# Performance work log

Measured on AMD Instinct MI355X. Metric: run time of the kernel, lower is better.

## Reference

```python
import jax, jax.numpy as jnp
import numpy as np

N_NODES = 100_000
N_EDGES = 1_600_000
HID = 64
TXT = 384
N_LAYERS = 2
BATCH = 1024


def setup_inputs() -> dict:
    key = jax.random.key(0)
    ks = jax.random.split(key, 13)
    s = 0.05
    return {
        "text_emb": jax.random.normal(ks[0], (N_NODES, TXT), dtype=jnp.float32),
        "weights": jax.random.uniform(ks[1], (N_EDGES,), dtype=jnp.float32),
        "W_enc": jax.random.normal(ks[2], (TXT, HID), dtype=jnp.float32) * s,
        "b_enc": jax.random.normal(ks[3], (HID,), dtype=jnp.float32) * s,
        "Wself_f": jax.random.normal(ks[4], (N_LAYERS, HID, HID), dtype=jnp.float32) * s,
        "Wneigh_f": jax.random.normal(ks[5], (N_LAYERS, HID, HID), dtype=jnp.float32) * s,
        "b_f": jax.random.normal(ks[6], (N_LAYERS, HID), dtype=jnp.float32) * s,
        "Wself_r": jax.random.normal(ks[7], (N_LAYERS, HID, HID), dtype=jnp.float32) * s,
        "Wneigh_r": jax.random.normal(ks[8], (N_LAYERS, HID, HID), dtype=jnp.float32) * s,
        "b_r": jax.random.normal(ks[9], (N_LAYERS, HID), dtype=jnp.float32) * s,
        "src": jax.random.randint(ks[10], (N_EDGES,), 0, N_NODES, dtype=jnp.int32),
        "dst": jax.random.randint(ks[11], (N_EDGES,), 0, N_NODES, dtype=jnp.int32),
        "ids_idx": jax.random.randint(ks[12], (BATCH,), 0, N_NODES, dtype=jnp.int32),
    }


def _inv_degree(idx, n, e_dtype):
    deg = jax.ops.segment_sum(jnp.ones((idx.shape[0],), dtype=e_dtype), idx, num_segments=n)
    return jnp.where(deg > 0, 1.0 / deg, 0.0)  # zero in-degree -> 0 (DGL mean)


def _sage_mean(x, src, dst, w, inv_deg, Wself, Wneigh, b):
    # DGL SAGEConv('mean') with edge_weight: neigh = mean_over_in_edges(w * h_src)
    m = w[:, None] * x[src]                                   # [E, H] gather
    neigh = jax.ops.segment_sum(m, dst, num_segments=x.shape[0]) * inv_deg[:, None]
    return x @ Wself + neigh @ Wneigh + b


def reference(text_emb, weights, W_enc, b_enc, Wself_f, Wneigh_f, b_f,
              Wself_r, Wneigh_r, b_r, src, dst, ids_idx):
    n = text_emb.shape[0]
    inv_f = _inv_degree(dst, n, text_emb.dtype)   # forward graph: aggregate into dst
    inv_r = _inv_degree(src, n, text_emb.dtype)   # reversed graph: aggregate into src
    x = text_emb @ W_enc + b_enc                  # text encoder
    for l in range(Wself_f.shape[0]):
        y = jax.nn.relu(_sage_mean(x, src, dst, weights, inv_f,
                                   Wself_f[l], Wneigh_f[l], b_f[l]))
        y = y + jax.nn.relu(_sage_mean(x, dst, src, weights, inv_r,
                                       Wself_r[l], Wneigh_r[l], b_r[l]))
        x = x + y                                 # skip connection
    feat = x[ids_idx]                             # [B, H]
    return feat / jnp.linalg.norm(feat, axis=1, keepdims=True)
```

## Files before the change

kernel.cpp:

```cpp
#include <hip/hip_runtime.h>

#define NN 100000
#define NE 1600000
#define HID 64
#define TXT 384
#define BATCH 1024
#define NBUCK 391
#define SBLK 256
#define EPB ((NE + SBLK - 1) / SBLK)
#define LDK2 72
#define EB2 782

typedef __attribute__((ext_vector_type(8))) short short8;
typedef __attribute__((ext_vector_type(4))) float float4v;

__device__ __forceinline__ ushort f2bf(float f) {
  unsigned u = __float_as_uint(f);
  unsigned r = (u + 0x7fffu + ((u >> 16) & 1u)) >> 16;
  return (ushort)r;
}
__device__ __forceinline__ float bf2f(ushort u) {
  return __uint_as_float(((unsigned)u) << 16);
}
__device__ __forceinline__ short8 pack8(float4 a, float4 b) {
  short8 s;
  s[0] = (short)f2bf(a.x); s[1] = (short)f2bf(a.y);
  s[2] = (short)f2bf(a.z); s[3] = (short)f2bf(a.w);
  s[4] = (short)f2bf(b.x); s[5] = (short)f2bf(b.y);
  s[6] = (short)f2bf(b.z); s[7] = (short)f2bf(b.w);
  return s;
}

__device__ __forceinline__ int scan_incl(int v, int* lds8) {
  const int lane = threadIdx.x & 63, wv = threadIdx.x >> 6;
  const int nw = blockDim.x >> 6;
  #pragma unroll
  for (int d = 1; d < 64; d <<= 1) {
    int t = __shfl_up(v, d);
    if (lane >= d) v += t;
  }
  if (lane == 63) lds8[wv] = v;
  __syncthreads();
  int add = 0;
  for (int i = 0; i < nw - 1; ++i)
    if (i < wv) add += lds8[i];
  __syncthreads();
  return v + add;
}

__global__ void k_init(const float* __restrict__ W, ushort* __restrict__ Wt,
                       unsigned char* __restrict__ idmap,
                       unsigned char* __restrict__ flag, int* __restrict__ nf) {
  const int b = blockIdx.x, t = threadIdx.x;
  if (b < 12) {
    const int unit = b * 4 + (t >> 6);
    const int lane = t & 63;
    const int ch = unit >> 2, nt = unit & 3;
    const int quad = lane >> 4, lr = lane & 15;
    short8 s;
    #pragma unroll
    for (int j = 0; j < 8; ++j)
      s[j] = (short)f2bf(W[(ch * 32 + quad * 8 + j) * 64 + nt * 16 + lr]);
    *(short8*)&Wt[((size_t)unit * 64 + lane) * 8] = s;
  } else {
    const int i = (b - 12) * 256 + t;
    if (i < NN / 4) { ((int*)idmap)[i] = 0; ((int*)flag)[i] = 0; }
    if (i == 0) *nf = 0;
  }
}

__global__ void k_seed(const int* __restrict__ ids,
                       unsigned char* __restrict__ idmap,
                       unsigned char* __restrict__ flag) {
  const int b = threadIdx.x;
  if (b < BATCH) { const int r = ids[b]; idmap[r] = 1; flag[r] = 1; }
}

__global__ void k_fedges(const int* __restrict__ src, const int* __restrict__ dst,
                         const unsigned char* __restrict__ idmap,
                         unsigned char* __restrict__ flag) {
  const int t = threadIdx.x, blk = blockIdx.x;
  const int e0 = blk * EPB, e1 = min(NE, e0 + EPB);
  for (int e = e0 + t; e < e1; e += 256) {
    const int s = src[e], d = dst[e];
    if (idmap[d]) flag[s] = 1;
    if (idmap[s]) flag[d] = 1;
  }
}

__launch_bounds__(256)
__global__ void k_mega(const float* __restrict__ T, const ushort* __restrict__ Wt,
                       const float* __restrict__ bias,
                       const unsigned char* __restrict__ flag,
                       float* __restrict__ x, ushort* __restrict__ xb,
                       const int* __restrict__ src, const int* __restrict__ dst,
                       int* __restrict__ cm_f, int* __restrict__ cm_r,
                       int* __restrict__ frows, int* __restrict__ nf) {
  __shared__ int hf[NBUCK], hr[NBUCK];
  const int bb = blockIdx.x;
  const int tid = threadIdx.x;
  if (bb < EB2) {
    const int row0 = bb * 128;
    const int wave = tid >> 6, lane = tid & 63;
    const int quad = lane >> 4, lr = lane & 15;
    const int rA = min(row0 + wave * 32 + lr, NN - 1);
    const int rB = min(row0 + wave * 32 + 16 + lr, NN - 1);
    const float* tpA = T + (size_t)rA * TXT + quad * 8;
    const float* tpB = T + (size_t)rB * TXT + quad * 8;
    const ushort* pw = Wt + lane * 8;

    float4 a0 = *(const float4*)(tpA);
    float4 a1 = *(const float4*)(tpA + 4);
    float4 b0 = *(const float4*)(tpB);
    float4 b1 = *(const float4*)(tpB + 4);
    float4v acc[2][4] = {};
    #pragma unroll
    for (int ch = 0; ch < 12; ++ch) {
      const short8 af0 = pack8(a0, a1);
      const short8 af1 = pack8(b0, b1);
      if (ch < 11) {
        const float* qa = tpA + (ch + 1) * 32;
        const float* qb = tpB + (ch + 1) * 32;
        a0 = *(const float4*)(qa); a1 = *(const float4*)(qa + 4);
        b0 = *(const float4*)(qb); b1 = *(const float4*)(qb + 4);
      }
      #pragma unroll
      for (int nt = 0; nt < 4; ++nt) {
        const short8 bfrag = *(const short8*)(pw + (size_t)(ch * 4 + nt) * 512);
        acc[0][nt] = __builtin_amdgcn_mfma_f32_16x16x32_bf16(af0, bfrag, acc[0][nt], 0, 0, 0);
        acc[1][nt] = __builtin_amdgcn_mfma_f32_16x16x32_bf16(af1, bfrag, acc[1][nt], 0, 0, 0);
      }
    }
    #pragma unroll
    for (int nt = 0; nt < 4; ++nt) {
      const int col = nt * 16 + lr;
      const float bcol = bias[col];
      #pragma unroll
      for (int mt = 0; mt < 2; ++mt) {
        #pragma unroll
        for (int r = 0; r < 4; ++r) {
          const int row = row0 + wave * 32 + mt * 16 + quad * 4 + r;
          if (row < NN) {
            const float v = acc[mt][nt][r] + bcol;
            const size_t idx = (size_t)row * 64 + col;
            xb[idx] = f2bf(v);
            if (flag[row]) x[idx] = v;
          }
        }
      }
    }
  } else if (bb < EB2 + SBLK) {
    const int blk = bb - EB2;
    for (int i = tid; i < NBUCK; i += 256) { hf[i] = 0; hr[i] = 0; }
    __syncthreads();
    const int e0 = blk * EPB, e1 = min(NE, e0 + EPB);
    for (int e = e0 + tid; e < e1; e += 256) {
      const int s = src[e], d = dst[e];
      if (flag[d]) atomicAdd(&hf[d >> 8], 1);
      if (flag[s]) atomicAdd(&hr[s >> 8], 1);
    }
    __syncthreads();
    for (int i = tid; i < NBUCK; i += 256) {
      cm_f[i * SBLK + blk] = hf[i];
      cm_r[i * SBLK + blk] = hr[i];
    }
  } else {
    const int i = (bb - EB2 - SBLK) * 256 + tid;
    if (i < NN && flag[i]) frows[atomicAdd(nf, 1)] = i;
  }
}

__global__ void k_scan1(int* __restrict__ cm_f, int* __restrict__ cm_r,
                        int* __restrict__ btot) {
  __shared__ int lds8[8];
  const int t = threadIdx.x;
  const int b = blockIdx.x;
  int* cm = (b < NBUCK) ? cm_f : cm_r;
  const int bucket = (b < NBUCK) ? b : b - NBUCK;
  int* row = cm + bucket * SBLK;
  const int v = row[t];
  const int incl = scan_incl(v, lds8);
  row[t] = incl - v;
  if (t == 255) btot[b] = incl;
}

__global__ void k_scan2(const int* __restrict__ btot,
                        int* __restrict__ bbase_f, int* __restrict__ bbase_r) {
  __shared__ int lds8[8];
  const int t = threadIdx.x;
  int h = (t < NBUCK) ? btot[t] : 0;
  int incl = scan_incl(h, lds8);
  if (t < NBUCK) bbase_f[t] = incl - h;
  h = (t < NBUCK) ? btot[NBUCK + t] : 0;
  incl = scan_incl(h, lds8);
  if (t < NBUCK) bbase_r[t] = incl - h;
}

__global__ void k_scatter2(const int* __restrict__ src, const int* __restrict__ dst,
                           const float* __restrict__ w,
                           const unsigned char* __restrict__ flag,
                           const int* __restrict__ cm_f, const int* __restrict__ cm_r,
                           const int* __restrict__ bbase_f, const int* __restrict__ bbase_r,
                           int2* __restrict__ stg_f, int2* __restrict__ stg_r) {
  __shared__ int cur_f[NBUCK], cur_r[NBUCK];
  const int t = threadIdx.x, blk = blockIdx.x;
  for (int i = t; i < NBUCK; i += 256) {
    cur_f[i] = bbase_f[i] + cm_f[i * SBLK + blk];
    cur_r[i] = bbase_r[i] + cm_r[i * SBLK + blk];
  }
  __syncthreads();
  const int e0 = blk * EPB, e1 = min(NE, e0 + EPB);
  for (int e = e0 + t; e < e1; e += 256) {
    const int s = src[e], d = dst[e];
    const int wb = __float_as_int(w[e]);
    if (flag[d]) {
      const int p = atomicAdd(&cur_f[d >> 8], 1);
      stg_f[p] = make_int2(((d & 255) << 24) | s, wb);
    }
    if (flag[s]) {
      const int q = atomicAdd(&cur_r[s >> 8], 1);
      stg_r[q] = make_int2(((s & 255) << 24) | d, wb);
    }
  }
}

__global__ void p_build(const unsigned char* __restrict__ flag,
                        const int2* __restrict__ stgf, const int* __restrict__ btotf,
                        const int* __restrict__ bbasef,
                        int* __restrict__ startf, int* __restrict__ cntf,
                        int2* __restrict__ cvf, int* __restrict__ permf,
                        const int2* __restrict__ stgr, const int* __restrict__ btotr,
                        const int* __restrict__ bbaser,
                        int* __restrict__ startr, int* __restrict__ cntr,
                        int2* __restrict__ cvr, int* __restrict__ permr) {
  int b = blockIdx.x;
  const int2* stg; const int* bcnt; const int* bbase;
  int* start; int* cnt; int2* cv; int* perm;
  if (b < NBUCK) { stg = stgf; bcnt = btotf; bbase = bbasef; start = startf; cnt = cntf; cv = cvf; perm = permf; }
  else { b -= NBUCK; stg = stgr; bcnt = btotr; bbase = bbaser; start = startr; cnt = cntr; cv = cvr; perm = permr; }
  const int base = bbase[b];
  const int n = bcnt[b];
  const int t = threadIdx.x;
  __shared__ int hist[256], cur[256], dh[256], dc[256], lds8[8];
  hist[t] = 0;
  perm[b * 256 + t] = -1;
  __syncthreads();
  for (int i = t; i < n; i += 256) {
    const unsigned pk = (unsigned)stg[base + i].x;
    atomicAdd(&hist[pk >> 24], 1);
  }
  __syncthreads();
  const int h = hist[t];
  const int excl = scan_incl(h, lds8) - h;
  const int node = (b << 8) + t;
  const bool valid = (node < NN) && flag[node];
  if (valid) { start[node] = base + excl; cnt[node] = h; }
  cur[t] = excl;
  dh[t] = 0; __syncthreads();
  const int dcap = min(h, 255);
  if (valid) atomicAdd(&dh[dcap], 1);
  __syncthreads();
  const int dv = dh[t];
  dc[t] = scan_incl(dv, lds8) - dv;
  __syncthreads();
  if (valid) {
    const int pos = atomicAdd(&dc[dcap], 1);
    perm[b * 256 + pos] = node;
  }
  __syncthreads();
  for (int i = t; i < n; i += 256) {
    const int2 en = stg[base + i];
    const unsigned d8 = ((unsigned)en.x) >> 24;
    const int pos = atomicAdd(&cur[d8], 1);
    cv[base + pos] = make_int2(en.x & 0xFFFFFF, en.y);
  }
}

__global__ void k_gather3(const ushort* __restrict__ xb,
                          const int* __restrict__ permf, const int* __restrict__ startf,
                          const int* __restrict__ cntf, const int2* __restrict__ cvf,
                          ushort* __restrict__ nbf,
                          const int* __restrict__ permr, const int* __restrict__ startr,
                          const int* __restrict__ cntr, const int2* __restrict__ cvr,
                          ushort* __restrict__ nbr) {
  const int BPD = (NBUCK * 256) / 16;
  int b = blockIdx.x;
  const int *perm, *start, *cnt; const int2* cv; ushort* outp;
  if (b < BPD) { perm = permf; start = startf; cnt = cntf; cv = cvf; outp = nbf; }
  else { b -= BPD; perm = permr; start = startr; cnt = cntr; cv = cvr; outp = nbr; }
  const int lane = threadIdx.x & 63;
  const int wave = threadIdx.x >> 6;
  const int slot = b * 16 + wave * 4 + (lane >> 4);
  const int fl = (lane & 15) * 4;
  const int row = perm[slot];
  if (row < 0) return;
  const int s = start[row], c = cnt[row];
  const int e = s + c;
  float a0 = 0.f, a1 = 0.f, a2 = 0.f, a3 = 0.f;
  int j = s;
  for (; j + 4 <= e; j += 4) {
    int2 e0 = cv[j], e1 = cv[j + 1], e2 = cv[j + 2], e3 = cv[j + 3];
    uint2 v0 = *(const uint2*)(xb + (size_t)e0.x * 64 + fl);
    uint2 v1 = *(const uint2*)(xb + (size_t)e1.x * 64 + fl);
    uint2 v2 = *(const uint2*)(xb + (size_t)e2.x * 64 + fl);
    uint2 v3 = *(const uint2*)(xb + (size_t)e3.x * 64 + fl);
    float w0 = __int_as_float(e0.y), w1 = __int_as_float(e1.y);
    float w2 = __int_as_float(e2.y), w3 = __int_as_float(e3.y);
    a0 += w0 * bf2f((ushort)v0.x); a1 += w0 * bf2f((ushort)(v0.x >> 16));
    a2 += w0 * bf2f((ushort)v0.y); a3 += w0 * bf2f((ushort)(v0.y >> 16));
    a0 += w1 * bf2f((ushort)v1.x); a1 += w1 * bf2f((ushort)(v1.x >> 16));
    a2 += w1 * bf2f((ushort)v1.y); a3 += w1 * bf2f((ushort)(v1.y >> 16));
    a0 += w2 * bf2f((ushort)v2.x); a1 += w2 * bf2f((ushort)(v2.x >> 16));
    a2 += w2 * bf2f((ushort)v2.y); a3 += w2 * bf2f((ushort)(v2.y >> 16));
    a0 += w3 * bf2f((ushort)v3.x); a1 += w3 * bf2f((ushort)(v3.x >> 16));
    a2 += w3 * bf2f((ushort)v3.y); a3 += w3 * bf2f((ushort)(v3.y >> 16));
  }
  for (; j < e; ++j) {
    int2 ee = cv[j];
    uint2 v = *(const uint2*)(xb + (size_t)ee.x * 64 + fl);
    float ww = __int_as_float(ee.y);
    a0 += ww * bf2f((ushort)v.x); a1 += ww * bf2f((ushort)(v.x >> 16));
    a2 += ww * bf2f((ushort)v.y); a3 += ww * bf2f((ushort)(v.y >> 16));
  }
  const float inv = (c > 0) ? 1.0f / (float)c : 0.f;
  uint2 pv;
  pv.x = (uint)f2bf(a0 * inv) | ((uint)f2bf(a1 * inv) << 16);
  pv.y = (uint)f2bf(a2 * inv) | ((uint)f2bf(a3 * inv) << 16);
  *(uint2*)(outp + (size_t)row * 64 + fl) = pv;
}

__global__ void k_bgather(const ushort* __restrict__ xb, const int* __restrict__ ids,
                          const int* __restrict__ startf, const int* __restrict__ cntf,
                          const int2* __restrict__ cvf, ushort* __restrict__ nbf,
                          const int* __restrict__ startr, const int* __restrict__ cntr,
                          const int2* __restrict__ cvr, ushort* __restrict__ nbr) {
  const int lane = threadIdx.x & 63;
  const int wave = threadIdx.x >> 6;
  const int fl = (lane & 15) * 4;
  const int t = blockIdx.x * 16 + wave * 4 + (lane >> 4);
  const int rev = (t >= BATCH);
  const int b = rev ? t - BATCH : t;
  const int row = ids[b];
  const int* start = rev ? startr : startf;
  const int* cnt   = rev ? cntr   : cntf;
  const int2* cv   = rev ? cvr    : cvf;
  ushort* outp     = rev ? nbr    : nbf;
  const int s = start[row], c = cnt[row];
  const int e = s + c;
  float a0 = 0.f, a1 = 0.f, a2 = 0.f, a3 = 0.f;
  int j = s;
  for (; j + 4 <= e; j += 4) {
    int2 e0 = cv[j], e1 = cv[j + 1], e2 = cv[j + 2], e3 = cv[j + 3];
    uint2 v0 = *(const uint2*)(xb + (size_t)e0.x * 64 + fl);
    uint2 v1 = *(const uint2*)(xb + (size_t)e1.x * 64 + fl);
    uint2 v2 = *(const uint2*)(xb + (size_t)e2.x * 64 + fl);
    uint2 v3 = *(const uint2*)(xb + (size_t)e3.x * 64 + fl);
    float w0 = __int_as_float(e0.y), w1 = __int_as_float(e1.y);
    float w2 = __int_as_float(e2.y), w3 = __int_as_float(e3.y);
    a0 += w0 * bf2f((ushort)v0.x); a1 += w0 * bf2f((ushort)(v0.x >> 16));
    a2 += w0 * bf2f((ushort)v0.y); a3 += w0 * bf2f((ushort)(v0.y >> 16));
    a0 += w1 * bf2f((ushort)v1.x); a1 += w1 * bf2f((ushort)(v1.x >> 16));
    a2 += w1 * bf2f((ushort)v1.y); a3 += w1 * bf2f((ushort)(v1.y >> 16));
    a0 += w2 * bf2f((ushort)v2.x); a1 += w2 * bf2f((ushort)(v2.x >> 16));
    a2 += w2 * bf2f((ushort)v2.y); a3 += w2 * bf2f((ushort)(v2.y >> 16));
    a0 += w3 * bf2f((ushort)v3.x); a1 += w3 * bf2f((ushort)(v3.x >> 16));
    a2 += w3 * bf2f((ushort)v3.y); a3 += w3 * bf2f((ushort)(v3.y >> 16));
  }
  for (; j < e; ++j) {
    int2 ee = cv[j];
    uint2 v = *(const uint2*)(xb + (size_t)ee.x * 64 + fl);
    float ww = __int_as_float(ee.y);
    a0 += ww * bf2f((ushort)v.x); a1 += ww * bf2f((ushort)(v.x >> 16));
    a2 += ww * bf2f((ushort)v.y); a3 += ww * bf2f((ushort)(v.y >> 16));
  }
  const float inv = (c > 0) ? 1.0f / (float)c : 0.f;
  uint2 pv;
  pv.x = (uint)f2bf(a0 * inv) | ((uint)f2bf(a1 * inv) << 16);
  pv.y = (uint)f2bf(a2 * inv) | ((uint)f2bf(a3 * inv) << 16);
  *(uint2*)(outp + (size_t)b * 64 + fl) = pv;
}

__launch_bounds__(256)
__global__ void k_layerf(const int* __restrict__ frows, const int* __restrict__ nfp,
                         const ushort* __restrict__ xbin,
                         const ushort* __restrict__ nbf, const ushort* __restrict__ nbr,
                         const float* __restrict__ Wsf, const float* __restrict__ Wnf,
                         const float* __restrict__ bfv,
                         const float* __restrict__ Wsr, const float* __restrict__ Wnr,
                         const float* __restrict__ brv,
                         float* __restrict__ x, ushort* __restrict__ xb) {
  const int nfv = *nfp;
  const int row0 = blockIdx.x * 128;
  if (row0 >= nfv) return;
  __shared__ short B4[4 * 64 * LDK2];
  __shared__ short As[128 * LDK2];
  const int tid = threadIdx.x;
  const int wave = tid >> 6, lane = tid & 63;
  const int quad = lane >> 4, lr = lane & 15;

  {
    #pragma unroll
    for (int j = 0; j < 16; ++j) {
      int idx = j * 256 + tid;
      int k = idx >> 6, n = idx & 63;
      B4[0 * 64 * LDK2 + n * LDK2 + k] = (short)f2bf(Wsf[idx]);
      B4[1 * 64 * LDK2 + n * LDK2 + k] = (short)f2bf(Wsr[idx]);
      B4[2 * 64 * LDK2 + n * LDK2 + k] = (short)f2bf(Wnf[idx]);
      B4[3 * 64 * LDK2 + n * LDK2 + k] = (short)f2bf(Wnr[idx]);
    }
  }
  const int srow = tid >> 1, half = (tid & 1) * 32;
  const int slot = row0 + srow;
  const int grow = frows[(slot < nfv) ? slot : 0];
  {
    const uint4* s = (const uint4*)(xbin + (size_t)grow * 64 + half);
    uint4* d = (uint4*)&As[srow * LDK2 + half];
    d[0] = s[0]; d[1] = s[1]; d[2] = s[2]; d[3] = s[3];
  }
  const uint4* pf = (const uint4*)(nbf + (size_t)grow * 64 + half);
  uint4 p0 = pf[0], p1 = pf[1], p2 = pf[2], p3 = pf[3];
  __syncthreads();

  float4v accf[2][4] = {}, accr[2][4] = {};
  #pragma unroll
  for (int kk = 0; kk < 64; kk += 32) {
    short8 a0 = *(const short8*)&As[(wave * 32 + lr) * LDK2 + kk + quad * 8];
    short8 a1 = *(const short8*)&As[(wave * 32 + 16 + lr) * LDK2 + kk + quad * 8];
    #pragma unroll
    for (int nt = 0; nt < 4; ++nt) {
      short8 bs = *(const short8*)&B4[0 * 64 * LDK2 + (nt * 16 + lr) * LDK2 + kk + quad * 8];
      accf[0][nt] = __builtin_amdgcn_mfma_f32_16x16x32_bf16(a0, bs, accf[0][nt], 0, 0, 0);
      accf[1][nt] = __builtin_amdgcn_mfma_f32_16x16x32_bf16(a1, bs, accf[1][nt], 0, 0, 0);
      short8 bq = *(const short8*)&B4[1 * 64 * LDK2 + (nt * 16 + lr) * LDK2 + kk + quad * 8];
      accr[0][nt] = __builtin_amdgcn_mfma_f32_16x16x32_bf16(a0, bq, accr[0][nt], 0, 0, 0);
      accr[1][nt] = __builtin_amdgcn_mfma_f32_16x16x32_bf16(a1, bq, accr[1][nt], 0, 0, 0);
    }
  }
  __syncthreads();
  { uint4* d = (uint4*)&As[srow * LDK2 + half]; d[0] = p0; d[1] = p1; d[2] = p2; d[3] = p3; }
  {
    const uint4* pr = (const uint4*)(nbr + (size_t)grow * 64 + half);
    p0 = pr[0]; p1 = pr[1]; p2 = pr[2]; p3 = pr[3];
  }
  __syncthreads();
  #pragma unroll
  for (int kk = 0; kk < 64; kk += 32) {
    short8 a0 = *(const short8*)&As[(wave * 32 + lr) * LDK2 + kk + quad * 8];
    short8 a1 = *(const short8*)&As[(wave * 32 + 16 + lr) * LDK2 + kk + quad * 8];
    #pragma unroll
    for (int nt = 0; nt < 4; ++nt) {
      short8 bs = *(const short8*)&B4[2 * 64 * LDK2 + (nt * 16 + lr) * LDK2 + kk + quad * 8];
      accf[0][nt] = __builtin_amdgcn_mfma_f32_16x16x32_bf16(a0, bs, accf[0][nt], 0, 0, 0);
      accf[1][nt] = __builtin_amdgcn_mfma_f32_16x16x32_bf16(a1, bs, accf[1][nt], 0, 0, 0);
    }
  }
  __syncthreads();
  { uint4* d = (uint4*)&As[srow * LDK2 + half]; d[0] = p0; d[1] = p1; d[2] = p2; d[3] = p3; }
  __syncthreads();
  #pragma unroll
  for (int kk = 0; kk < 64; kk += 32) {
    short8 a0 = *(const short8*)&As[(wave * 32 + lr) * LDK2 + kk + quad * 8];
    short8 a1 = *(const short8*)&As[(wave * 32 + 16 + lr) * LDK2 + kk + quad * 8];
    #pragma unroll
    for (int nt = 0; nt < 4; ++nt) {
      short8 bs = *(const short8*)&B4[3 * 64 * LDK2 + (nt * 16 + lr) * LDK2 + kk + quad * 8];
      accr[0][nt] = __builtin_amdgcn_mfma_f32_16x16x32_bf16(a0, bs, accr[0][nt], 0, 0, 0);
      accr[1][nt] = __builtin_amdgcn_mfma_f32_16x16x32_bf16(a1, bs, accr[1][nt], 0, 0, 0);
    }
  }
  #pragma unroll
  for (int nt = 0; nt < 4; ++nt) {
    const int col = nt * 16 + lr;
    const float bf_c = bfv[col], br_c = brv[col];
    #pragma unroll
    for (int mt = 0; mt < 2; ++mt) {
      #pragma unroll
      for (int r = 0; r < 4; ++r) {
        const int rl = wave * 32 + mt * 16 + quad * 4 + r;
        const int slotE = row0 + rl;
        if (slotE < nfv) {
          const int node = frows[slotE];
          const size_t idx = (size_t)node * 64 + col;
          const float v = x[idx] + fmaxf(accf[mt][nt][r] + bf_c, 0.f)
                                 + fmaxf(accr[mt][nt][r] + br_c, 0.f);
          x[idx] = v;
          xb[idx] = f2bf(v);
        }
      }
    }
  }
}

__launch_bounds__(256)
__global__ void k_blayer(const ushort* __restrict__ xbin, const float* __restrict__ x,
                         const int* __restrict__ ids,
                         const ushort* __restrict__ nbf, const ushort* __restrict__ nbr,
                         const float* __restrict__ Wsf, const float* __restrict__ Wnf,
                         const float* __restrict__ bfv,
                         const float* __restrict__ Wsr, const float* __restrict__ Wnr,
                         const float* __restrict__ brv,
                         float* __restrict__ out) {
  __shared__ short B4[4 * 64 * LDK2];
  __shared__ short As[128 * LDK2];
  const int tid = threadIdx.x;
  const int b0 = blockIdx.x * 128;
  const int wave = tid >> 6, lane = tid & 63;
  const int quad = lane >> 4, lr = lane & 15;

  #pragma unroll
  for (int j = 0; j < 16; ++j) {
    int idx = j * 256 + tid;
    int k = idx >> 6, n = idx & 63;
    B4[0 * 64 * LDK2 + n * LDK2 + k] = (short)f2bf(Wsf[idx]);
    B4[1 * 64 * LDK2 + n * LDK2 + k] = (short)f2bf(Wsr[idx]);
    B4[2 * 64 * LDK2 + n * LDK2 + k] = (short)f2bf(Wnf[idx]);
    B4[3 * 64 * LDK2 + n * LDK2 + k] = (short)f2bf(Wnr[idx]);
  }
  const int srow = tid >> 1, half = (tid & 1) * 32;
  const int node0 = ids[b0 + srow];
  {
    const uint4* s = (const uint4*)(xbin + (size_t)node0 * 64 + half);
    uint4* d = (uint4*)&As[srow * LDK2 + half];
    d[0] = s[0]; d[1] = s[1]; d[2] = s[2]; d[3] = s[3];
  }
  __syncthreads();

  float4v accf[2][4] = {}, accr[2][4] = {};
  #pragma unroll
  for (int kk = 0; kk < 64; kk += 32) {
    short8 a0 = *(const short8*)&As[(wave * 32 + lr) * LDK2 + kk + quad * 8];
    short8 a1 = *(const short8*)&As[(wave * 32 + 16 + lr) * LDK2 + kk + quad * 8];
    #pragma unroll
    for (int nt = 0; nt < 4; ++nt) {
      short8 bs = *(const short8*)&B4[0 * 64 * LDK2 + (nt * 16 + lr) * LDK2 + kk + quad * 8];
      accf[0][nt] = __builtin_amdgcn_mfma_f32_16x16x32_bf16(a0, bs, accf[0][nt], 0, 0, 0);
      accf[1][nt] = __builtin_amdgcn_mfma_f32_16x16x32_bf16(a1, bs, accf[1][nt], 0, 0, 0);
      short8 bq = *(const short8*)&B4[1 * 64 * LDK2 + (nt * 16 + lr) * LDK2 + kk + quad * 8];
      accr[0][nt] = __builtin_amdgcn_mfma_f32_16x16x32_bf16(a0, bq, accr[0][nt], 0, 0, 0);
      accr[1][nt] = __builtin_amdgcn_mfma_f32_16x16x32_bf16(a1, bq, accr[1][nt], 0, 0, 0);
    }
  }
  __syncthreads();
  {
    const uint4* s = (const uint4*)(nbf + (size_t)(b0 + srow) * 64 + half);
    uint4* d = (uint4*)&As[srow * LDK2 + half];
    d[0] = s[0]; d[1] = s[1]; d[2] = s[2]; d[3] = s[3];
  }
  __syncthreads();
  #pragma unroll
  for (int kk = 0; kk < 64; kk += 32) {
    short8 a0 = *(const short8*)&As[(wave * 32 + lr) * LDK2 + kk + quad * 8];
    short8 a1 = *(const short8*)&As[(wave * 32 + 16 + lr) * LDK2 + kk + quad * 8];
    #pragma unroll
    for (int nt = 0; nt < 4; ++nt) {
      short8 bs = *(const short8*)&B4[2 * 64 * LDK2 + (nt * 16 + lr) * LDK2 + kk + quad * 8];
      accf[0][nt] = __builtin_amdgcn_mfma_f32_16x16x32_bf16(a0, bs, accf[0][nt], 0, 0, 0);
      accf[1][nt] = __builtin_amdgcn_mfma_f32_16x16x32_bf16(a1, bs, accf[1][nt], 0, 0, 0);
    }
  }
  __syncthreads();
  {
    const uint4* s = (const uint4*)(nbr + (size_t)(b0 + srow) * 64 + half);
    uint4* d = (uint4*)&As[srow * LDK2 + half];
    d[0] = s[0]; d[1] = s[1]; d[2] = s[2]; d[3] = s[3];
  }
  __syncthreads();
  #pragma unroll
  for (int kk = 0; kk < 64; kk += 32) {
    short8 a0 = *(const short8*)&As[(wave * 32 + lr) * LDK2 + kk + quad * 8];
    short8 a1 = *(const short8*)&As[(wave * 32 + 16 + lr) * LDK2 + kk + quad * 8];
    #pragma unroll
    for (int nt = 0; nt < 4; ++nt) {
      short8 bs = *(const short8*)&B4[3 * 64 * LDK2 + (nt * 16 + lr) * LDK2 + kk + quad * 8];
      accr[0][nt] = __builtin_amdgcn_mfma_f32_16x16x32_bf16(a0, bs, accr[0][nt], 0, 0, 0);
      accr[1][nt] = __builtin_amdgcn_mfma_f32_16x16x32_bf16(a1, bs, accr[1][nt], 0, 0, 0);
    }
  }
  float vv[2][4][4];
  #pragma unroll
  for (int nt = 0; nt < 4; ++nt) {
    const int col = nt * 16 + lr;
    const float bf_c = bfv[col], br_c = brv[col];
    #pragma unroll
    for (int mt = 0; mt < 2; ++mt) {
      #pragma unroll
      for (int r = 0; r < 4; ++r) {
        const int rl = wave * 32 + mt * 16 + quad * 4 + r;
        const int node = ids[b0 + rl];
        vv[mt][nt][r] = x[(size_t)node * 64 + col]
                      + fmaxf(accf[mt][nt][r] + bf_c, 0.f)
                      + fmaxf(accr[mt][nt][r] + br_c, 0.f);
      }
    }
  }
  #pragma unroll
  for (int mt = 0; mt < 2; ++mt) {
    #pragma unroll
    for (int r = 0; r < 4; ++r) {
      float s = 0.f;
      #pragma unroll
      for (int nt = 0; nt < 4; ++nt) s += vv[mt][nt][r] * vv[mt][nt][r];
      s += __shfl_xor(s, 1); s += __shfl_xor(s, 2);
      s += __shfl_xor(s, 4); s += __shfl_xor(s, 8);
      const int rl = wave * 32 + mt * 16 + quad * 4 + r;
      const float inv = 1.f / sqrtf(s);
      #pragma unroll
      for (int nt = 0; nt < 4; ++nt)
        out[(size_t)(b0 + rl) * 64 + nt * 16 + lr] = vv[mt][nt][r] * inv;
    }
  }
}

extern "C" void kernel_launch(void* const* d_in, const int* in_sizes, int n_in,
                              void* d_out, int out_size, void* d_ws, size_t ws_size,
                              hipStream_t stream) {
  const float* text = (const float*)d_in[0];
  const float* wts  = (const float*)d_in[1];
  const float* Wenc = (const float*)d_in[2];
  const float* benc = (const float*)d_in[3];
  const float* Wsf  = (const float*)d_in[4];
  const float* Wnf  = (const float*)d_in[5];
  const float* bf   = (const float*)d_in[6];
  const float* Wsr  = (const float*)d_in[7];
  const float* Wnr  = (const float*)d_in[8];
  const float* br   = (const float*)d_in[9];
  const int*   src  = (const int*)d_in[10];
  const int*   dst  = (const int*)d_in[11];
  const int*   ids  = (const int*)d_in[12];
  float* out = (float*)d_out;

  char* ws = (char*)d_ws;
  size_t o = 0;
  auto alloc = [&](size_t f32elems) {
    void* p = ws + o;
    o += f32elems * 4;
    o = (o + 255) & ~(size_t)255;
    return p;
  };
  float*  x   = (float*)alloc((size_t)NN * 64);
  ushort* xb  = (ushort*)alloc((size_t)NN * 32);
  ushort* nbf = (ushort*)alloc((size_t)NN * 32);
  ushort* nbr = (ushort*)alloc((size_t)NN * 32);
  ushort* Wt  = (ushort*)alloc(48 * 512 / 2);
  int2*   cvf = (int2*)alloc((size_t)NE * 2);
  int2*   cvr = (int2*)alloc((size_t)NE * 2);
  int* cm_f    = (int*)alloc((size_t)NBUCK * SBLK);
  int* cm_r    = (int*)alloc((size_t)NBUCK * SBLK);
  int* btot    = (int*)alloc(2 * NBUCK);
  int* bbase_f = (int*)alloc(NBUCK);
  int* bbase_r = (int*)alloc(NBUCK);
  int* startf  = (int*)alloc(NN);
  int* cntf    = (int*)alloc(NN);
  int* startr  = (int*)alloc(NN);
  int* cntr    = (int*)alloc(NN);
  int* permf   = (int*)alloc((size_t)NBUCK * 256);
  int* permr   = (int*)alloc((size_t)NBUCK * 256);
  unsigned char* idmap = (unsigned char*)alloc(NN / 4 + 64);
  unsigned char* flag  = (unsigned char*)alloc(NN / 4 + 64);
  int* frows = (int*)alloc(NN);
  int* nf    = (int*)alloc(64);

  int2* stg_f = (int2*)nbf;
  int2* stg_r = (int2*)nbr;

  k_init<<<12 + 98, 256, 0, stream>>>(Wenc, Wt, idmap, flag, nf);
  k_seed<<<1, 1024, 0, stream>>>(ids, idmap, flag);
  k_fedges<<<SBLK, 256, 0, stream>>>(src, dst, idmap, flag);
  k_mega<<<EB2 + SBLK + 391, 256, 0, stream>>>(text, Wt, benc, flag, x, xb,
                                               src, dst, cm_f, cm_r, frows, nf);
  k_scan1<<<2 * NBUCK, 256, 0, stream>>>(cm_f, cm_r, btot);
  k_scan2<<<1, 512, 0, stream>>>(btot, bbase_f, bbase_r);
  k_scatter2<<<SBLK, 256, 0, stream>>>(src, dst, wts, flag, cm_f, cm_r,
                                       bbase_f, bbase_r, stg_f, stg_r);
  p_build<<<2 * NBUCK, 256, 0, stream>>>(flag,
                                         stg_f, btot, bbase_f, startf, cntf, cvf, permf,
                                         stg_r, btot + NBUCK, bbase_r, startr, cntr, cvr, permr);
  const int GB3 = 2 * ((NBUCK * 256) / 16);
  k_gather3<<<GB3, 256, 0, stream>>>(xb, permf, startf, cntf, cvf, nbf,
                                     permr, startr, cntr, cvr, nbr);
  k_layerf<<<EB2, 256, 0, stream>>>(frows, nf, xb, nbf, nbr,
                                    Wsf, Wnf, bf, Wsr, Wnr, br, x, xb);
  k_bgather<<<(2 * BATCH) / 16, 256, 0, stream>>>(xb, ids, startf, cntf, cvf, nbf,
                                                  startr, cntr, cvr, nbr);
  k_blayer<<<BATCH / 128, 256, 0, stream>>>(xb, x, ids, nbf, nbr,
                                            Wsf + HID * HID, Wnf + HID * HID, bf + HID,
                                            Wsr + HID * HID, Wnr + HID * HID, br + HID,
                                            out);
}
```

Before: 458.9 us.

## Use 512-thread blocks in k_mega with one row tile per wave and int2 edge loads

k_mega now launches 512-thread blocks. In the encoder GEMM part, each of the 8 waves computes one 16-row MFMA tile, where before each of 4 waves computed two tiles. This trades per-wave ILP for more waves in flight to hide the latency of the global text loads. The histogram part reads src/dst as int2 pairs with 512 threads, and the compaction part covers 512 nodes per block with a smaller grid. Fewer accumulators lower register pressure, but there are fewer independent MFMA chains per wave.

```diff
diff --git a/kernel.cpp b/kernel.cpp
--- a/kernel.cpp
+++ b/kernel.cpp
@@ -10,6 +10,7 @@
 #define EPB ((NE + SBLK - 1) / SBLK)
 #define LDK2 72
 #define EB2 782
+#define CPB 196
 
 typedef __attribute__((ext_vector_type(8))) short short8;
 typedef __attribute__((ext_vector_type(4))) float float4v;
@@ -88,7 +89,7 @@
   }
 }
 
-__launch_bounds__(256)
+__launch_bounds__(512)
 __global__ void k_mega(const float* __restrict__ T, const ushort* __restrict__ Wt,
                        const float* __restrict__ bias,
                        const unsigned char* __restrict__ flag,
@@ -103,32 +104,24 @@
     const int row0 = bb * 128;
     const int wave = tid >> 6, lane = tid & 63;
     const int quad = lane >> 4, lr = lane & 15;
-    const int rA = min(row0 + wave * 32 + lr, NN - 1);
-    const int rB = min(row0 + wave * 32 + 16 + lr, NN - 1);
-    const float* tpA = T + (size_t)rA * TXT + quad * 8;
-    const float* tpB = T + (size_t)rB * TXT + quad * 8;
+    const int rW = min(row0 + wave * 16 + lr, NN - 1);
+    const float* tp = T + (size_t)rW * TXT + quad * 8;
     const ushort* pw = Wt + lane * 8;
 
-    float4 a0 = *(const float4*)(tpA);
-    float4 a1 = *(const float4*)(tpA + 4);
-    float4 b0 = *(const float4*)(tpB);
-    float4 b1 = *(const float4*)(tpB + 4);
-    float4v acc[2][4] = {};
+    float4 a0 = *(const float4*)(tp);
+    float4 a1 = *(const float4*)(tp + 4);
+    float4v acc[4] = {};
     #pragma unroll
     for (int ch = 0; ch < 12; ++ch) {
-      const short8 af0 = pack8(a0, a1);
-      const short8 af1 = pack8(b0, b1);
+      const short8 af = pack8(a0, a1);
       if (ch < 11) {
-        const float* qa = tpA + (ch + 1) * 32;
-        const float* qb = tpB + (ch + 1) * 32;
-        a0 = *(const float4*)(qa); a1 = *(const float4*)(qa + 4);
-        b0 = *(const float4*)(qb); b1 = *(const float4*)(qb + 4);
+        const float* q = tp + (ch + 1) * 32;
+        a0 = *(const float4*)(q); a1 = *(const float4*)(q + 4);
       }
       #pragma unroll
       for (int nt = 0; nt < 4; ++nt) {
         const short8 bfrag = *(const short8*)(pw + (size_t)(ch * 4 + nt) * 512);
-        acc[0][nt] = __builtin_amdgcn_mfma_f32_16x16x32_bf16(af0, bfrag, acc[0][nt], 0, 0, 0);
-        acc[1][nt] = __builtin_amdgcn_mfma_f32_16x16x32_bf16(af1, bfrag, acc[1][nt], 0, 0, 0);
+        acc[nt] = __builtin_amdgcn_mfma_f32_16x16x32_bf16(af, bfrag, acc[nt], 0, 0, 0);
       }
     }
     #pragma unroll
@@ -136,36 +129,38 @@
       const int col = nt * 16 + lr;
       const float bcol = bias[col];
       #pragma unroll
-      for (int mt = 0; mt < 2; ++mt) {
-        #pragma unroll
-        for (int r = 0; r < 4; ++r) {
-          const int row = row0 + wave * 32 + mt * 16 + quad * 4 + r;
-          if (row < NN) {
-            const float v = acc[mt][nt][r] + bcol;
-            const size_t idx = (size_t)row * 64 + col;
-            xb[idx] = f2bf(v);
-            if (flag[row]) x[idx] = v;
-          }
+      for (int r = 0; r < 4; ++r) {
+        const int row = row0 + wave * 16 + quad * 4 + r;
+        if (row < NN) {
+          const float v = acc[nt][r] + bcol;
+          const size_t idx = (size_t)row * 64 + col;
+          xb[idx] = f2bf(v);
+          if (flag[row]) x[idx] = v;
         }
       }
     }
   } else if (bb < EB2 + SBLK) {
     const int blk = bb - EB2;
-    for (int i = tid; i < NBUCK; i += 256) { hf[i] = 0; hr[i] = 0; }
+    for (int i = tid; i < NBUCK; i += 512) { hf[i] = 0; hr[i] = 0; }
     __syncthreads();
-    const int e0 = blk * EPB, e1 = min(NE, e0 + EPB);
-    for (int e = e0 + tid; e < e1; e += 256) {
-      const int s = src[e], d = dst[e];
-      if (flag[d]) atomicAdd(&hf[d >> 8], 1);
-      if (flag[s]) atomicAdd(&hr[s >> 8], 1);
+    const int p0 = blk * (EPB / 2);
+    const int2* sp = (const int2*)src;
+    const int2* dp = (const int2*)dst;
+    for (int i = tid; i < EPB / 2; i += 512) {
+      const int2 ss = sp[p0 + i];
+      const int2 dd = dp[p0 + i];
+      if (flag[dd.x]) atomicAdd(&hf[dd.x >> 8], 1);
+      if (flag[ss.x]) atomicAdd(&hr[ss.x >> 8], 1);
+      if (flag[dd.y]) atomicAdd(&hf[dd.y >> 8], 1);
+      if (flag[ss.y]) atomicAdd(&hr[ss.y >> 8], 1);
     }
     __syncthreads();
-    for (int i = tid; i < NBUCK; i += 256) {
+    for (int i = tid; i < NBUCK; i += 512) {
       cm_f[i * SBLK + blk] = hf[i];
       cm_r[i * SBLK + blk] = hr[i];
     }
   } else {
-    const int i = (bb - EB2 - SBLK) * 256 + tid;
+    const int i = (bb - EB2 - SBLK) * 512 + tid;
     if (i < NN && flag[i]) frows[atomicAdd(nf, 1)] = i;
   }
 }
@@ -666,7 +661,7 @@
   k_init<<<12 + 98, 256, 0, stream>>>(Wenc, Wt, idmap, flag, nf);
   k_seed<<<1, 1024, 0, stream>>>(ids, idmap, flag);
   k_fedges<<<SBLK, 256, 0, stream>>>(src, dst, idmap, flag);
-  k_mega<<<EB2 + SBLK + 391, 256, 0, stream>>>(text, Wt, benc, flag, x, xb,
+  k_mega<<<EB2 + SBLK + CPB, 512, 0, stream>>>(text, Wt, benc, flag, x, xb,
                                                src, dst, cm_f, cm_r, frows, nf);
   k_scan1<<<2 * NBUCK, 256, 0, stream>>>(cm_f, cm_r, btot);
   k_scan2<<<1, 512, 0, stream>>>(btot, bbase_f, bbase_r);
```

Result: no change. 460.2 us (+0.3%).
